# Performance work log

Hardware: AMD Instinct MI355X
Metric: run time of the kernel (lower is better)

The kernel has to match this reference:

```python
import jax, jax.numpy as jnp
import numpy as np

B, T, E, H = 8, 2048, 1024, 128

def setup_inputs() -> dict:
    key = jax.random.key(0)
    kx, kq, kk, kv = jax.random.split(key, 4)
    x = jax.random.normal(kx, (B, T, E), dtype=jnp.float32)
    # Linear(E, H, bias=False) weights, stored as (E, H) so y = x @ W
    s = 1.0 / np.sqrt(E)
    Wq = jax.random.normal(kq, (E, H), dtype=jnp.float32) * s
    Wk = jax.random.normal(kk, (E, H), dtype=jnp.float32) * s
    Wv = jax.random.normal(kv, (E, H), dtype=jnp.float32) * s
    return {"x": x, "Wq": Wq, "Wk": Wk, "Wv": Wv}

def reference(x, Wq, Wk, Wv):
    # x: (B, T, E)
    Tcur = x.shape[1]
    q = jnp.einsum('bte,eh->bth', x, Wq)
    k = jnp.einsum('bte,eh->bth', x, Wk)
    v = jnp.einsum('bte,eh->bth', x, Wv)
    scores = jnp.einsum('bqh,bkh->bqk', q, k)  # (B, T, T)
    # NOTE: source multiplies by x.shape[2]**0.5 where x.shape[2] == T here
    scores = scores * jnp.sqrt(jnp.asarray(Tcur, dtype=scores.dtype))
    causal = jnp.tril(jnp.ones((Tcur, Tcur), dtype=bool))
    scores = jnp.where(causal, scores, -jnp.inf)
    attn = jax.nn.softmax(scores, axis=2)
    # dropout p=0.0 -> identity
    return jnp.einsum('bqk,bkh->bqh', attn, v)
```

## Files before the change

### kernel.cpp

```cpp
#include <hip/hip_runtime.h>
#include <hip/hip_bf16.h>
#include <math.h>

#define B_ 8
#define T_ 2048
#define E_ 1024
#define H_ 128
#define M_ (B_*T_)
#define SCALE_ 45.25483399593904f
#define SEG_ 4

typedef __attribute__((ext_vector_type(8))) short bf16x8;
typedef __attribute__((ext_vector_type(4))) float f32x4;

#define mfma16(A, Bv, C) __builtin_amdgcn_mfma_f32_16x16x32_bf16((A), (Bv), (C), 0, 0, 0)

#define FRAGW(g, kc, lane)  ((((size_t)(g)*32 + (kc))*64 + (lane))*8)
#define FRAGK(b, kt16, kc, lane) (((((size_t)(b)*128 + (kt16))*4 + (kc))*64 + (lane))*8)
#define FRAGV(b, ht, kt32, lane) (((((size_t)(b)*8 + (ht))*64 + (kt32))*64 + (lane))*8)

__device__ __forceinline__ ushort bf16_rne(float f) {
  unsigned u = __float_as_uint(f);
  u += 0x7fffu + ((u >> 16) & 1u);
  return (ushort)(u >> 16);
}
__device__ __forceinline__ float bf16_tof(ushort h) {
  return __uint_as_float(((unsigned)h) << 16);
}

__device__ __forceinline__ void lds_barrier() {
  asm volatile("s_waitcnt lgkmcnt(0)" ::: "memory");
  __builtin_amdgcn_s_barrier();
}

template <int N>
__device__ __forceinline__ float ror16(float x) {
  return __uint_as_float((unsigned)__builtin_amdgcn_update_dpp(
      0, (int)__float_as_uint(x), 0x120 + N, 0xF, 0xF, true));
}
__device__ __forceinline__ float rowmax16(float x) {
  x = fmaxf(x, ror16<8>(x));
  x = fmaxf(x, ror16<4>(x));
  x = fmaxf(x, ror16<2>(x));
  x = fmaxf(x, ror16<1>(x));
  return x;
}
__device__ __forceinline__ float rowsum16(float x) {
  x += ror16<8>(x);
  x += ror16<4>(x);
  x += ror16<2>(x);
  x += ror16<1>(x);
  return x;
}

__global__ __launch_bounds__(256) void wsplit(
    const float* __restrict__ Wq, const float* __restrict__ Wk,
    const float* __restrict__ Wv,
    ushort* __restrict__ whT, ushort* __restrict__ wlT)
{
  const int idx  = blockIdx.x * 256 + threadIdx.x;
  const int mat  = idx >> 14;
  const int rem  = idx & 16383;
  const int nt   = rem >> 11;
  const int kc   = (rem >> 6) & 31;
  const int lane = rem & 63;
  const int quad = lane >> 4, l15 = lane & 15;
  const float* W = (mat == 0) ? Wq : (mat == 1) ? Wk : Wv;
  const int n  = nt * 16 + l15;
  const int k0 = kc * 32 + quad * 8;
  bf16x8 hv, lv;
  #pragma unroll
  for (int j = 0; j < 8; ++j) {
    const float f = W[(size_t)(k0 + j) * H_ + n];
    const ushort h = bf16_rne(f);
    hv[j] = (short)h;
    lv[j] = (short)bf16_rne(f - bf16_tof(h));
  }
  *(bf16x8*)(whT + (size_t)idx * 8) = hv;
  *(bf16x8*)(wlT + (size_t)idx * 8) = lv;
}

#define CVT8W(F0, F1, DSTOFF) do {                                            \
    const float f_[8] = {(F0).x, (F0).y, (F0).z, (F0).w,                      \
                         (F1).x, (F1).y, (F1).z, (F1).w};                     \
    bf16x8 hv_, lv_;                                                          \
    _Pragma("unroll")                                                         \
    for (int jj_ = 0; jj_ < 8; ++jj_) {                                       \
      const ushort h_ = bf16_rne(f_[jj_]);                                    \
      hv_[jj_] = (short)h_;                                                   \
      lv_[jj_] = (short)bf16_rne(f_[jj_] - bf16_tof(h_));                     \
    }                                                                         \
    *(bf16x8*)&SM[(DSTOFF) + ca * 8] = hv_;                                   \
    *(bf16x8*)&SM[(DSTOFF) + 2048 + ca * 8] = lv_;                            \
  } while (0)

#define PSTEP4(S, CUR, NXT, BHC, BLC, BHN, BLN) do {                          \
    bf16x8 ah_[4], al_[4];                                                    \
    _Pragma("unroll")                                                         \
    for (int mt_ = 0; mt_ < 4; ++mt_) {                                       \
      ah_[mt_] = *(const bf16x8*)                                             \
          &SM[(CUR)*8192 + (((mt_*4 + quad)*16) + l15)*8];                    \
      al_[mt_] = *(const bf16x8*)                                             \
          &SM[(CUR)*8192 + 2048 + (((mt_*4 + quad)*16) + l15)*8];             \
    }                                                                         \
    if ((S) + 1 < 16) {                                                       \
      _Pragma("unroll")                                                       \
      for (int kch_ = 0; kch_ < 2; ++kch_) {                                  \
        const int kcn_ = 2*((S)+1) + kch_;                                    \
        BHN[kch_*3+0] = *(const bf16x8*)(whT + FRAGW(gq,     kcn_, lane));    \
        BHN[kch_*3+1] = *(const bf16x8*)(whT + FRAGW(gq + 4, kcn_, lane));    \
        BHN[kch_*3+2] = *(const bf16x8*)(whT + FRAGW(gv,     kcn_, lane));    \
        BLN[kch_*2+0] = *(const bf16x8*)(wlT + FRAGW(gq,     kcn_, lane));    \
        BLN[kch_*2+1] = *(const bf16x8*)(wlT + FRAGW(gq + 4, kcn_, lane));    \
      }                                                                       \
    }                                                                         \
    float4 nx0_, nx1_, nx2_, nx3_;                                            \
    if ((S) + 2 < 16) {                                                       \
      nx0_ = *(const float4*)(xrow + 64*((S)+2));                             \
      nx1_ = *(const float4*)(xrow + 64*((S)+2) + 4);                         \
      nx2_ = *(const float4*)(xrow + 64*((S)+2) + 32);                        \
      nx3_ = *(const float4*)(xrow + 64*((S)+2) + 36);                        \
    } else { nx0_ = xf0; nx1_ = xf1; nx2_ = xf2; nx3_ = xf3; }                \
                                                     \
    _Pragma("unroll")                                                         \
    for (int mt_ = 0; mt_ < 4; ++mt_) {                                       \
      acc[0][mt_] = mfma16(ah_[mt_], BHC[0], acc[0][mt_]);                    \
      acc[0][mt_] = mfma16(ah_[mt_], BLC[0], acc[0][mt_]);                    \
      acc[0][mt_] = mfma16(al_[mt_], BHC[0], acc[0][mt_]);                    \
      acc[1][mt_] = mfma16(ah_[mt_], BHC[1], acc[1][mt_]);                    \
      acc[1][mt_] = mfma16(ah_[mt_], BLC[1], acc[1][mt_]);                    \
      acc[1][mt_] = mfma16(al_[mt_], BHC[1], acc[1][mt_]);                    \
      acc[2][mt_] = mfma16(ah_[mt_], BHC[2], acc[2][mt_]);                    \
    }                                                                         \
                                            \
    if ((S) + 1 < 16) {                                                       \
      CVT8W(xf0, xf1, (NXT)*8192);                                            \
      CVT8W(xf2, xf3, (NXT)*8192 + 4096);                                     \
    }                                                                         \
                                                \
    _Pragma("unroll")                                                         \
    for (int mt_ = 0; mt_ < 4; ++mt_) {                                       \
      ah_[mt_] = *(const bf16x8*)                                             \
          &SM[(CUR)*8192 + 4096 + (((mt_*4 + quad)*16) + l15)*8];             \
      al_[mt_] = *(const bf16x8*)                                             \
          &SM[(CUR)*8192 + 6144 + (((mt_*4 + quad)*16) + l15)*8];             \
    }                                                                         \
    _Pragma("unroll")                                                         \
    for (int mt_ = 0; mt_ < 4; ++mt_) {                                       \
      acc[0][mt_] = mfma16(ah_[mt_], BHC[3], acc[0][mt_]);                    \
      acc[0][mt_] = mfma16(ah_[mt_], BLC[2], acc[0][mt_]);                    \
      acc[0][mt_] = mfma16(al_[mt_], BHC[3], acc[0][mt_]);                    \
      acc[1][mt_] = mfma16(ah_[mt_], BHC[4], acc[1][mt_]);                    \
      acc[1][mt_] = mfma16(ah_[mt_], BLC[3], acc[1][mt_]);                    \
      acc[1][mt_] = mfma16(al_[mt_], BHC[4], acc[1][mt_]);                    \
      acc[2][mt_] = mfma16(ah_[mt_], BHC[5], acc[2][mt_]);                    \
    }                                                                         \
    xf0 = nx0_; xf1 = nx1_; xf2 = nx2_; xf3 = nx3_;                           \
    lds_barrier();                                                            \
  } while (0)

__global__ __launch_bounds__(256, 2) void proj_fused(
    const float* __restrict__ x,
    const ushort* __restrict__ whT, const ushort* __restrict__ wlT,
    ushort* __restrict__ qh, ushort* __restrict__ ql,
    ushort* __restrict__ kfh, ushort* __restrict__ kfl,
    ushort* __restrict__ vF)
{
  const int m0   = blockIdx.x * 64;
  const int half = blockIdx.y;
  const int tid  = threadIdx.x;
  const int wave = tid >> 6, lane = tid & 63;
  const int quad = lane >> 4, l15 = lane & 15;

  __shared__ __align__(16) ushort SM[16384];

  f32x4 acc[3][4];
  #pragma unroll
  for (int j = 0; j < 3; ++j)
    #pragma unroll
    for (int mt = 0; mt < 4; ++mt) acc[j][mt] = (f32x4){0.f, 0.f, 0.f, 0.f};

  const int arow  = tid >> 2;
  const int akoff = (tid & 3) * 8;
  const int ca    = ((arow >> 4) * 4 + (tid & 3)) * 16 + (arow & 15);
  const int gq    = half * 8 + wave;
  const int gv    = 16 + half * 4 + wave;

  const float* xrow = x + (size_t)(m0 + arow) * E_ + akoff;

  float4 xf0, xf1, xf2, xf3;
  bf16x8 bhA[6], blA[4], bhB[6], blB[4];

  {
    const float4 a0 = *(const float4*)(xrow);
    const float4 a1 = *(const float4*)(xrow + 4);
    const float4 a2 = *(const float4*)(xrow + 32);
    const float4 a3 = *(const float4*)(xrow + 36);
    CVT8W(a0, a1, 0);
    CVT8W(a2, a3, 4096);
    xf0 = *(const float4*)(xrow + 64);
    xf1 = *(const float4*)(xrow + 68);
    xf2 = *(const float4*)(xrow + 96);
    xf3 = *(const float4*)(xrow + 100);
    #pragma unroll
    for (int kch = 0; kch < 2; ++kch) {
      bhA[kch*3+0] = *(const bf16x8*)(whT + FRAGW(gq,     kch, lane));
      bhA[kch*3+1] = *(const bf16x8*)(whT + FRAGW(gq + 4, kch, lane));
      bhA[kch*3+2] = *(const bf16x8*)(whT + FRAGW(gv,     kch, lane));
      blA[kch*2+0] = *(const bf16x8*)(wlT + FRAGW(gq,     kch, lane));
      blA[kch*2+1] = *(const bf16x8*)(wlT + FRAGW(gq + 4, kch, lane));
    }
  }
  lds_barrier();

  int s = 0;
  while (true) {
    PSTEP4(s, 0, 1, bhA, blA, bhB, blB); if (++s == 16) break;
    PSTEP4(s, 1, 0, bhB, blB, bhA, blA); if (++s == 16) break;
  }

  #pragma unroll
  for (int j = 0; j < 2; ++j) {
    const int g = gq + 4 * j;
    if (half == 0) {
      const int ncol = g * 16 + l15;
      #pragma unroll
      for (int mt = 0; mt < 4; ++mt)
        #pragma unroll
        for (int r = 0; r < 4; ++r) {
          const float a = acc[j][mt][r];
          const ushort h = bf16_rne(a);
          const size_t off = (size_t)(m0 + mt * 16 + quad * 4 + r) * H_ + ncol;
          qh[off] = h;
          ql[off] = bf16_rne(a - bf16_tof(h));
        }
    } else {
      const int hcol = (g - 8) * 16 + l15;
      const int kch  = hcol >> 5;
      const int qdh  = (hcol >> 3) & 3;
      const int jj   = hcol & 7;
      #pragma unroll
      for (int mt = 0; mt < 4; ++mt)
        #pragma unroll
        for (int r = 0; r < 4; ++r) {
          const float a = acc[j][mt][r];
          const int tg = m0 + mt * 16 + quad * 4 + r;
          const int bb = tg >> 11, tl = tg & 2047;
          const size_t ad = FRAGK(bb, tl >> 4, kch, qdh * 16 + (tl & 15)) + jj;
          const ushort h = bf16_rne(a);
          kfh[ad] = h;
          kfl[ad] = bf16_rne(a - bf16_tof(h));
        }
    }
  }
  __syncthreads();
  {
    ushort* smT = SM;
    const int lh = wave * 16 + l15;
    #pragma unroll
    for (int mt = 0; mt < 4; ++mt)
      #pragma unroll
      for (int r = 0; r < 4; ++r)
        smT[lh * 72 + mt * 16 + quad * 4 + r] = bf16_rne(acc[2][mt][r]);
    __syncthreads();
    const int bb = m0 >> 11, t0 = m0 & 2047;
    #pragma unroll
    for (int u = 0; u < 2; ++u) {
      const int c    = u * 256 + tid;
      const int lht  = c >> 7;
      const int ktl  = (c >> 6) & 1;
      const int lv   = c & 63;
      const int qv   = lv >> 4, l15v = lv & 15;
      *(bf16x8*)(vF + FRAGV(bb, half * 4 + lht, (t0 >> 5) + ktl, lv)) =
          *(const bf16x8*)&smT[(lht * 16 + l15v) * 72 + ktl * 32 + qv * 8];
    }
  }
}

__global__ __launch_bounds__(256) void attn_flash(
    const ushort* __restrict__ qh, const ushort* __restrict__ ql,
    const ushort* __restrict__ kfh, const ushort* __restrict__ kfl,
    const ushort* __restrict__ vF,
    ushort* __restrict__ Opart, float* __restrict__ mlpart)
{
  const int b    = (int)blockIdx.x & 7;
  const int seg  = (int)blockIdx.x >> 3;
  const int qt   = 31 - (int)blockIdx.y;
  const int q0   = qt * 64;
  const int tid  = threadIdx.x;
  const int wave = tid >> 6, lane = tid & 63;
  const int quad = lane >> 4, l15 = lane & 15;
  const f32x4 z4 = (f32x4){0.f, 0.f, 0.f, 0.f};

  __shared__ __align__(16) ushort KhS[4096];
  __shared__ __align__(16) ushort KlS[4096];
  __shared__ __align__(16) ushort VtS[4096];
  __shared__ __align__(16) ushort smP[4 * 640];

  const int ntiles = 2 * qt + 2;
  const int cnt    = (ntiles + SEG_ - 1) >> 2;
  const int jt0    = seg * cnt;
  const int jt1    = (jt0 + cnt < ntiles) ? (jt0 + cnt) : ntiles;

  const int q0w = q0 + wave * 16;
  const int ntw = ((q0w + 15) >> 5) + 1;
  const size_t pidx = ((size_t)(b * 128 + qt * 4 + wave)) * SEG_ + seg;
  ushort* op = Opart + pidx * 2048;
  float*  ml = mlpart + pidx * 32;

  if (jt0 >= jt1) {
    const bf16x8 zz = {0, 0, 0, 0, 0, 0, 0, 0};
    #pragma unroll
    for (int u = 0; u < 4; ++u)
      *(bf16x8*)(op + lane * 32 + u * 8) = zz;
    if (lane < 32) ml[lane] = (lane & 1) ? 0.f : -1e30f;
    return;
  }

  const size_t base = (size_t)b * T_ * H_;

  const ushort* qhp = qh + base + (size_t)(q0w + l15) * H_ + quad * 8;
  const ushort* qlp = ql + base + (size_t)(q0w + l15) * H_ + quad * 8;
  bf16x8 Qh[4], Ql[4];
  #pragma unroll
  for (int c = 0; c < 4; ++c) {
    Qh[c] = *(const bf16x8*)(qhp + c * 32);
    Ql[c] = *(const bf16x8*)(qlp + c * 32);
  }

  f32x4 O[8];
  #pragma unroll
  for (int i = 0; i < 8; ++i) O[i] = z4;
  float mstate[4] = {-1e30f, -1e30f, -1e30f, -1e30f};
  float lstate[4] = {0.f, 0.f, 0.f, 0.f};

  bf16x8 rkh[2], rkl[2], rv[2];
  {
    #pragma unroll
    for (int u = 0; u < 2; ++u) {
      const int c = u * 256 + tid;
      rkh[u] = *(const bf16x8*)(kfh + FRAGK(b, 2 * jt0 + (c >> 8), (c >> 6) & 3, c & 63));
      rkl[u] = *(const bf16x8*)(kfl + FRAGK(b, 2 * jt0 + (c >> 8), (c >> 6) & 3, c & 63));
      rv[u]  = *(const bf16x8*)(vF  + FRAGV(b, c >> 6, jt0, c & 63));
    }
  }

  for (int jt = jt0; jt < jt1; ++jt) {
    __syncthreads();
    #pragma unroll
    for (int u = 0; u < 2; ++u) {
      const int c = u * 256 + tid;
      *(bf16x8*)&KhS[c * 8] = rkh[u];
      *(bf16x8*)&KlS[c * 8] = rkl[u];
      *(bf16x8*)&VtS[c * 8] = rv[u];
    }
    __syncthreads();

    if (jt + 1 < jt1) {
      #pragma unroll
      for (int u = 0; u < 2; ++u) {
        const int c = u * 256 + tid;
        rkh[u] = *(const bf16x8*)(kfh + FRAGK(b, 2 * (jt + 1) + (c >> 8), (c >> 6) & 3, c & 63));
        rkl[u] = *(const bf16x8*)(kfl + FRAGK(b, 2 * (jt + 1) + (c >> 8), (c >> 6) & 3, c & 63));
        rv[u]  = *(const bf16x8*)(vF  + FRAGV(b, c >> 6, jt + 1, c & 63));
      }
    }

    if (jt < ntw) {
      const int k0 = jt * 32;
      f32x4 shh0 = z4, shh1 = z4, sx0 = z4, sx1 = z4;
      #pragma unroll
      for (int c = 0; c < 4; ++c) {
        const bf16x8 kh0 = *(const bf16x8*)&KhS[(c * 64 + lane) * 8];
        const bf16x8 kh1 = *(const bf16x8*)&KhS[((4 + c) * 64 + lane) * 8];
        const bf16x8 kl0 = *(const bf16x8*)&KlS[(c * 64 + lane) * 8];
        const bf16x8 kl1 = *(const bf16x8*)&KlS[((4 + c) * 64 + lane) * 8];
        shh0 = mfma16(Qh[c], kh0, shh0);
        shh1 = mfma16(Qh[c], kh1, shh1);
        sx0  = mfma16(Qh[c], kl0, sx0);
        sx1  = mfma16(Qh[c], kl1, sx1);
        sx0  = mfma16(Ql[c], kh0, sx0);
        sx1  = mfma16(Ql[c], kh1, sx1);
      }

      float s0[4], s1[4];
      #pragma unroll
      for (int r = 0; r < 4; ++r) {
        s0[r] = (shh0[r] + sx0[r]) * SCALE_;
        s1[r] = (shh1[r] + sx1[r]) * SCALE_;
      }
      if (jt == ntw - 1) {
        const int krel0 = k0 + l15      - q0w - quad * 4;
        const int krel1 = k0 + 16 + l15 - q0w - quad * 4;
        #pragma unroll
        for (int r = 0; r < 4; ++r) {
          if (krel0 > r) s0[r] = -1e30f;
          if (krel1 > r) s1[r] = -1e30f;
        }
      }

      float alpha[4];
      #pragma unroll
      for (int r = 0; r < 4; ++r) {
        const float rm   = rowmax16(fmaxf(s0[r], s1[r]));
        const float mnew = fmaxf(mstate[r], rm);
        alpha[r] = __expf(mstate[r] - mnew);
        mstate[r] = mnew;
        const float p0 = __expf(s0[r] - mnew);
        const float p1 = __expf(s1[r] - mnew);
        lstate[r] = lstate[r] * alpha[r] + rowsum16(p0 + p1);
        smP[wave * 640 + (quad * 4 + r) * 40 + l15]      = bf16_rne(p0);
        smP[wave * 640 + (quad * 4 + r) * 40 + 16 + l15] = bf16_rne(p1);
      }
      #pragma unroll
      for (int ct = 0; ct < 8; ++ct) {
        O[ct][0] *= alpha[0]; O[ct][1] *= alpha[1];
        O[ct][2] *= alpha[2]; O[ct][3] *= alpha[3];
      }
      const bf16x8 pA = *(const bf16x8*)&smP[wave * 640 + l15 * 40 + quad * 8];
      #pragma unroll
      for (int ct = 0; ct < 8; ++ct) {
        const bf16x8 vf = *(const bf16x8*)&VtS[(ct * 64 + lane) * 8];
        O[ct] = mfma16(pA, vf, O[ct]);
      }
    }
  }

  #pragma unroll
  for (int r = 0; r < 4; ++r)
    #pragma unroll
    for (int ct = 0; ct < 8; ++ct)
      op[(quad * 4 + r) * 128 + ct * 16 + l15] = bf16_rne(O[ct][r]);
  if (l15 == 0) {
    #pragma unroll
    for (int r = 0; r < 4; ++r) {
      ml[(quad * 4 + r) * 2]     = mstate[r];
      ml[(quad * 4 + r) * 2 + 1] = lstate[r];
    }
  }
}

__global__ __launch_bounds__(256) void attn_combine(
    const ushort* __restrict__ Opart, const float* __restrict__ mlpart,
    float* __restrict__ out)
{
  const int idx = blockIdx.x * 256 + threadIdx.x;
  const int c4  = idx & 31;
  const int r   = idx >> 5;
  const int t   = r & 2047;
  const int qt  = t >> 4, r16 = t & 15;
  const size_t pb = ((size_t)((r >> 11) * 128 + qt)) * SEG_;

  float m[SEG_], l[SEG_];
  #pragma unroll
  for (int s = 0; s < SEG_; ++s) {
    m[s] = mlpart[(pb + s) * 32 + r16 * 2];
    l[s] = mlpart[(pb + s) * 32 + r16 * 2 + 1];
  }
  float M = m[0];
  #pragma unroll
  for (int s = 1; s < SEG_; ++s) M = fmaxf(M, m[s]);
  float w[SEG_], L = 0.f;
  #pragma unroll
  for (int s = 0; s < SEG_; ++s) {
    w[s] = __expf(m[s] - M);
    L += l[s] * w[s];
  }
  float4 acc = make_float4(0.f, 0.f, 0.f, 0.f);
  #pragma unroll
  for (int s = 0; s < SEG_; ++s) {
    const ushort4 o = *(const ushort4*)(Opart + (pb + s) * 2048 + r16 * 128 + c4 * 4);
    acc.x += w[s] * bf16_tof(o.x);
    acc.y += w[s] * bf16_tof(o.y);
    acc.z += w[s] * bf16_tof(o.z);
    acc.w += w[s] * bf16_tof(o.w);
  }
  const float inv = 1.0f / L;
  *(float4*)(out + (size_t)r * H_ + c4 * 4) =
      make_float4(acc.x * inv, acc.y * inv, acc.z * inv, acc.w * inv);
}

extern "C" void kernel_launch(void* const* d_in, const int* in_sizes, int n_in,
                              void* d_out, int out_size, void* d_ws, size_t ws_size,
                              hipStream_t stream) {
  (void)in_sizes; (void)n_in; (void)out_size; (void)ws_size;
  const float* x  = (const float*)d_in[0];
  const float* Wq = (const float*)d_in[1];
  const float* Wk = (const float*)d_in[2];
  const float* Wv = (const float*)d_in[3];
  float* out = (float*)d_out;

  ushort* qhb = (ushort*)d_ws;
  ushort* qlb = qhb + (size_t)M_ * H_;
  ushort* kfh = qlb + (size_t)M_ * H_;
  ushort* kfl = kfh + (size_t)M_ * H_;
  ushort* vFb = kfl + (size_t)M_ * H_;
  ushort* whT = vFb + (size_t)M_ * H_;
  ushort* wlT = whT + (size_t)3 * H_ * E_;
  ushort* Opart = wlT + (size_t)3 * H_ * E_;
  float*  mlpart = (float*)(Opart + (size_t)B_ * 128 * SEG_ * 2048);

  wsplit<<<dim3(192), 256, 0, stream>>>(Wq, Wk, Wv, whT, wlT);
  proj_fused<<<dim3(M_/64, 2), 256, 0, stream>>>(x, whT, wlT,
                                                 qhb, qlb, kfh, kfl, vFb);
  attn_flash<<<dim3(B_*SEG_, 32), 256, 0, stream>>>(qhb, qlb, kfh, kfl, vFb,
                                                    Opart, mlpart);
  attn_combine<<<dim3(2048), 256, 0, stream>>>(Opart, mlpart, out);
}
```

Before: 174.3 us.

## Transpose attention MFMA so each lane owns one query row

Swaps the MFMA operand order so the score and output tiles come out transposed, with each lane holding one query row. The row max and row sum then become local reductions plus two cross-lane shuffles instead of DPP row reductions, and the per-row softmax state shrinks to a single scalar. The scale factor is folded into the exponent, P is written to LDS as packed 64-bit words, and the partial O is staged through LDS so the global stores are coalesced 16-byte writes. The cost is an extra __syncthreads and LDS round trip at the epilogue, plus more complex indexing.

Measured after the change: 170.4 us. 2.3% less time.

```diff
diff --git a/kernel.cpp b/kernel.cpp
--- a/kernel.cpp
+++ b/kernel.cpp
@@ -31,26 +31,6 @@
 __device__ __forceinline__ void lds_barrier() {
   asm volatile("s_waitcnt lgkmcnt(0)" ::: "memory");
   __builtin_amdgcn_s_barrier();
-}
-
-template <int N>
-__device__ __forceinline__ float ror16(float x) {
-  return __uint_as_float((unsigned)__builtin_amdgcn_update_dpp(
-      0, (int)__float_as_uint(x), 0x120 + N, 0xF, 0xF, true));
-}
-__device__ __forceinline__ float rowmax16(float x) {
-  x = fmaxf(x, ror16<8>(x));
-  x = fmaxf(x, ror16<4>(x));
-  x = fmaxf(x, ror16<2>(x));
-  x = fmaxf(x, ror16<1>(x));
-  return x;
-}
-__device__ __forceinline__ float rowsum16(float x) {
-  x += ror16<8>(x);
-  x += ror16<4>(x);
-  x += ror16<2>(x);
-  x += ror16<1>(x);
-  return x;
 }
 
 __global__ __launch_bounds__(256) void wsplit(
@@ -292,10 +272,12 @@
   const int quad = lane >> 4, l15 = lane & 15;
   const f32x4 z4 = (f32x4){0.f, 0.f, 0.f, 0.f};
 
-  __shared__ __align__(16) ushort KhS[4096];
-  __shared__ __align__(16) ushort KlS[4096];
-  __shared__ __align__(16) ushort VtS[4096];
-  __shared__ __align__(16) ushort smP[4 * 640];
+  __shared__ __align__(16) ushort SMa[12288];
+  __shared__ __align__(16) unsigned smPw[1280];
+  ushort* KhS = SMa;
+  ushort* KlS = SMa + 4096;
+  ushort* VtS = SMa + 8192;
+  unsigned* pw = smPw + wave * 320;
 
   const int ntiles = 2 * qt + 2;
   const int cnt    = (ntiles + SEG_ - 1) >> 2;
@@ -331,8 +313,8 @@
   f32x4 O[8];
   #pragma unroll
   for (int i = 0; i < 8; ++i) O[i] = z4;
-  float mstate[4] = {-1e30f, -1e30f, -1e30f, -1e30f};
-  float lstate[4] = {0.f, 0.f, 0.f, 0.f};
+  float mst = -1e30f;
+  float lst = 0.f;
 
   bf16x8 rkh[2], rkl[2], rv[2];
   {
@@ -375,68 +357,91 @@
         const bf16x8 kh1 = *(const bf16x8*)&KhS[((4 + c) * 64 + lane) * 8];
         const bf16x8 kl0 = *(const bf16x8*)&KlS[(c * 64 + lane) * 8];
         const bf16x8 kl1 = *(const bf16x8*)&KlS[((4 + c) * 64 + lane) * 8];
-        shh0 = mfma16(Qh[c], kh0, shh0);
-        shh1 = mfma16(Qh[c], kh1, shh1);
-        sx0  = mfma16(Qh[c], kl0, sx0);
-        sx1  = mfma16(Qh[c], kl1, sx1);
-        sx0  = mfma16(Ql[c], kh0, sx0);
-        sx1  = mfma16(Ql[c], kh1, sx1);
-      }
-
-      float s0[4], s1[4];
+        shh0 = mfma16(kh0, Qh[c], shh0);
+        shh1 = mfma16(kh1, Qh[c], shh1);
+        sx0  = mfma16(kl0, Qh[c], sx0);
+        sx1  = mfma16(kl1, Qh[c], sx1);
+        sx0  = mfma16(kh0, Ql[c], sx0);
+        sx1  = mfma16(kh1, Ql[c], sx1);
+      }
+
+      float r0[4], r1[4];
       #pragma unroll
       for (int r = 0; r < 4; ++r) {
-        s0[r] = (shh0[r] + sx0[r]) * SCALE_;
-        s1[r] = (shh1[r] + sx1[r]) * SCALE_;
+        r0[r] = shh0[r] + sx0[r];
+        r1[r] = shh1[r] + sx1[r];
       }
       if (jt == ntw - 1) {
-        const int krel0 = k0 + l15      - q0w - quad * 4;
-        const int krel1 = k0 + 16 + l15 - q0w - quad * 4;
+        const int base0 = q0w + l15 - k0 - quad * 4;
         #pragma unroll
         for (int r = 0; r < 4; ++r) {
-          if (krel0 > r) s0[r] = -1e30f;
-          if (krel1 > r) s1[r] = -1e30f;
+          if (r > base0)      r0[r] = -1e30f;
+          if (r > base0 - 16) r1[r] = -1e30f;
         }
       }
 
-      float alpha[4];
+      float pm = fmaxf(fmaxf(fmaxf(r0[0], r0[1]), fmaxf(r0[2], r0[3])),
+                       fmaxf(fmaxf(r1[0], r1[1]), fmaxf(r1[2], r1[3])));
+      pm = fmaxf(pm, __shfl_xor(pm, 16));
+      pm = fmaxf(pm, __shfl_xor(pm, 32));
+
+      const float mnew  = fmaxf(mst, pm);
+      const float alpha = __expf((mst - mnew) * SCALE_);
+      mst = mnew;
+
+      float p0[4], p1[4];
       #pragma unroll
       for (int r = 0; r < 4; ++r) {
-        const float rm   = rowmax16(fmaxf(s0[r], s1[r]));
-        const float mnew = fmaxf(mstate[r], rm);
-        alpha[r] = __expf(mstate[r] - mnew);
-        mstate[r] = mnew;
-        const float p0 = __expf(s0[r] - mnew);
-        const float p1 = __expf(s1[r] - mnew);
-        lstate[r] = lstate[r] * alpha[r] + rowsum16(p0 + p1);
-        smP[wave * 640 + (quad * 4 + r) * 40 + l15]      = bf16_rne(p0);
-        smP[wave * 640 + (quad * 4 + r) * 40 + 16 + l15] = bf16_rne(p1);
-      }
+        p0[r] = __expf((r0[r] - mnew) * SCALE_);
+        p1[r] = __expf((r1[r] - mnew) * SCALE_);
+      }
+      float sm = ((p0[0] + p0[1]) + (p0[2] + p0[3])) +
+                 ((p1[0] + p1[1]) + (p1[2] + p1[3]));
+      sm += __shfl_xor(sm, 16);
+      sm += __shfl_xor(sm, 32);
+      lst = lst * alpha + sm;
+
+      const unsigned w0 = (unsigned)bf16_rne(p0[0]) | ((unsigned)bf16_rne(p0[1]) << 16);
+      const unsigned w1 = (unsigned)bf16_rne(p0[2]) | ((unsigned)bf16_rne(p0[3]) << 16);
+      const unsigned w2 = (unsigned)bf16_rne(p1[0]) | ((unsigned)bf16_rne(p1[1]) << 16);
+      const unsigned w3 = (unsigned)bf16_rne(p1[2]) | ((unsigned)bf16_rne(p1[3]) << 16);
+      *(unsigned long long*)&pw[l15 * 20 + 2 * quad] =
+          (unsigned long long)w0 | ((unsigned long long)w1 << 32);
+      *(unsigned long long*)&pw[l15 * 20 + 8 + 2 * quad] =
+          (unsigned long long)w2 | ((unsigned long long)w3 << 32);
+
       #pragma unroll
       for (int ct = 0; ct < 8; ++ct) {
-        O[ct][0] *= alpha[0]; O[ct][1] *= alpha[1];
-        O[ct][2] *= alpha[2]; O[ct][3] *= alpha[3];
-      }
-      const bf16x8 pA = *(const bf16x8*)&smP[wave * 640 + l15 * 40 + quad * 8];
+        O[ct][0] *= alpha; O[ct][1] *= alpha;
+        O[ct][2] *= alpha; O[ct][3] *= alpha;
+      }
+      const bf16x8 pB = *(const bf16x8*)&pw[l15 * 20 + 4 * quad];
       #pragma unroll
       for (int ct = 0; ct < 8; ++ct) {
         const bf16x8 vf = *(const bf16x8*)&VtS[(ct * 64 + lane) * 8];
-        O[ct] = mfma16(pA, vf, O[ct]);
-      }
-    }
-  }
-
-  #pragma unroll
-  for (int r = 0; r < 4; ++r)
+        O[ct] = mfma16(vf, pB, O[ct]);
+      }
+    }
+  }
+
+  __syncthreads();
+  {
+    ushort* smO = SMa + wave * 2176;
     #pragma unroll
     for (int ct = 0; ct < 8; ++ct)
-      op[(quad * 4 + r) * 128 + ct * 16 + l15] = bf16_rne(O[ct][r]);
-  if (l15 == 0) {
-    #pragma unroll
-    for (int r = 0; r < 4; ++r) {
-      ml[(quad * 4 + r) * 2]     = mstate[r];
-      ml[(quad * 4 + r) * 2 + 1] = lstate[r];
-    }
+      #pragma unroll
+      for (int r = 0; r < 4; ++r)
+        smO[l15 * 136 + ct * 16 + quad * 4 + r] = bf16_rne(O[ct][r]);
+    #pragma unroll
+    for (int u = 0; u < 4; ++u) {
+      const int q_ = u * 4 + quad;
+      *(bf16x8*)(op + q_ * 128 + l15 * 8) =
+          *(const bf16x8*)&smO[q_ * 136 + l15 * 8];
+    }
+  }
+  if (quad == 0) {
+    ml[l15 * 2]     = mst * SCALE_;
+    ml[l15 * 2 + 1] = lst;
   }
 }
 
```
